# Performance work log

Measured on AMD Instinct MI355X. Metric: run time of the kernel, lower is better.

## Reference

```python
import jax, jax.numpy as jnp
import numpy as np

B, N, D = 8, 512, 768
HS = 64          # gp_head_size
NT = 12          # len(tag_vocab)
NEG = 1e12


def setup_inputs() -> dict:
    key = jax.random.key(0)
    ks = jax.random.split(key, 14)
    s = 0.02  # init scale for weights
    return {
        "chars": jax.random.normal(ks[0], (B, N, D), dtype=jnp.float32),
        "mask": jax.random.randint(ks[1], (B, N), 0, 2).astype(jnp.int32),
        "w1_ent": jax.random.normal(ks[2], (2 * HS, D), dtype=jnp.float32) * s,
        "b1_ent": jax.random.normal(ks[3], (2 * HS,), dtype=jnp.float32) * s,
        "w2_ent": jax.random.normal(ks[4], (2 * 2, 2 * HS), dtype=jnp.float32) * s,
        "b2_ent": jax.random.normal(ks[5], (2 * 2,), dtype=jnp.float32) * s,
        "w1_head": jax.random.normal(ks[6], (2 * HS, D), dtype=jnp.float32) * s,
        "b1_head": jax.random.normal(ks[7], (2 * HS,), dtype=jnp.float32) * s,
        "w2_head": jax.random.normal(ks[8], (2 * NT, 2 * HS), dtype=jnp.float32) * s,
        "b2_head": jax.random.normal(ks[9], (2 * NT,), dtype=jnp.float32) * s,
        "w1_tail": jax.random.normal(ks[10], (2 * HS, D), dtype=jnp.float32) * s,
        "b1_tail": jax.random.normal(ks[11], (2 * HS,), dtype=jnp.float32) * s,
        "w2_tail": jax.random.normal(ks[12], (2 * NT, 2 * HS), dtype=jnp.float32) * s,
        "b2_tail": jax.random.normal(ks[13], (2 * NT,), dtype=jnp.float32) * s,
    }


def _egp(x, w1, b1, w2, b2, mask, head_size, rope, tril):
    # x: [B,N,D] -> h: [B,N,2*head_size]
    h = jnp.einsum('bnd,ed->bne', x, w1) + b1
    qw, kw = h[..., 0::2], h[..., 1::2]          # [B,N,head_size] each
    if rope:
        n = x.shape[1]
        pos = jnp.arange(n, dtype=x.dtype)
        inv = jnp.power(10000.0, -2.0 * jnp.arange(head_size // 2, dtype=x.dtype) / head_size)
        ang = pos[:, None] * inv[None, :]         # [N, head_size/2]
        cos = jnp.repeat(jnp.cos(ang), 2, axis=-1)[None]  # [1,N,head_size]
        sin = jnp.repeat(jnp.sin(ang), 2, axis=-1)[None]
        def rot(t):
            t2 = jnp.stack([-t[..., 1::2], t[..., 0::2]], axis=-1).reshape(t.shape)
            return t * cos + t2 * sin
        qw, kw = rot(qw), rot(kw)
    logits = jnp.einsum('bmd,bnd->bmn', qw, kw) / (head_size ** 0.5)  # [B,M,N]
    bias = (jnp.einsum('bne,he->bnh', h, w2) + b2).transpose(0, 2, 1) / 2.0  # [B,2H,N]
    # [B,H,M,N]
    logits = logits[:, None] + bias[:, 0::2, None, :] + bias[:, 1::2, :, None]
    m = mask.astype(logits.dtype)
    pad = 1.0 - m[:, None, None, :] * m[:, None, :, None]
    logits = logits - pad * NEG
    if tril:
        tri = jnp.tril(jnp.ones((logits.shape[-2], logits.shape[-1]), logits.dtype), k=-1)
        logits = logits - tri * NEG
    return logits


def reference(chars, mask, w1_ent, b1_ent, w2_ent, b2_ent,
              w1_head, b1_head, w2_head, b2_head,
              w1_tail, b1_tail, w2_tail, b2_tail):
    entity = _egp(chars, w1_ent, b1_ent, w2_ent, b2_ent, mask, HS, True, True)
    head = _egp(chars, w1_head, b1_head, w2_head, b2_head, mask, HS, False, False)
    tail = _egp(chars, w1_tail, b1_tail, w2_tail, b2_tail, mask, HS, False, False)
    return (entity, head, tail)
```

## Files before the change

kernel.cpp:

```cpp
#include <hip/hip_runtime.h>
#include <cstddef>

namespace {
constexpr int B_ = 8;
constexpr int N_ = 512;
constexpr int D_ = 768;
constexpr int HS_ = 64;
constexpr int M_ = B_ * N_;
constexpr int E_ = 2 * HS_;
constexpr float NEGV = 1000000000000.0f;
constexpr float LOG2_10000 = 13.287712379549449f;
}

typedef short mfrag_t __attribute__((ext_vector_type(8)));
typedef float macc_t  __attribute__((ext_vector_type(4)));

__device__ __forceinline__ unsigned short bft(float x) {
    union { float f; unsigned u; } c; c.f = x;
    return (unsigned short)(c.u >> 16);
}
__device__ __forceinline__ unsigned short bfrne(float x) {
    union { float f; unsigned u; } c; c.f = x;
    const unsigned r = c.u + 0x7FFFu + ((c.u >> 16) & 1u);
    return (unsigned short)(r >> 16);
}

__global__ __launch_bounds__(256) void prep_kernel(
    const float* __restrict__ chars,
    const float* __restrict__ w1e, const float* __restrict__ b1e,
    const float* __restrict__ w2e, const float* __restrict__ b2e,
    const float* __restrict__ w1h, const float* __restrict__ b1h,
    const float* __restrict__ w2h, const float* __restrict__ b2h,
    const float* __restrict__ w1t, const float* __restrict__ b1t,
    const float* __restrict__ w2t, const float* __restrict__ b2t,
    unsigned short* __restrict__ qbf, unsigned short* __restrict__ kbf,
    float* __restrict__ bias_e, float* __restrict__ bias_h, float* __restrict__ bias_t)
{
    const int fam = blockIdx.y;
    const float* w1 = (fam == 0) ? w1e : (fam == 1) ? w1h : w1t;
    const float* b1 = (fam == 0) ? b1e : (fam == 1) ? b1h : b1t;
    const float* w2 = (fam == 0) ? w2e : (fam == 1) ? w2h : w2t;
    const float* b2 = (fam == 0) ? b2e : (fam == 1) ? b2h : b2t;
    float* bout = (fam == 0) ? bias_e : (fam == 1) ? bias_h : bias_t;
    const int H2 = (fam == 0) ? 4 : 24;
    unsigned short* qout = qbf + (size_t)fam * M_ * HS_;
    unsigned short* kout = kbf + (size_t)fam * M_ * HS_;
    const int m0 = blockIdx.x * 64;

    __shared__ unsigned short A_lds[64][40];
    __shared__ unsigned short B_lds[128][40];
    __shared__ float hs[64][132];

    const int t    = threadIdx.x;
    const int w    = t >> 6;
    const int lane = t & 63;
    const int ml   = lane & 15;
    const int quad = lane >> 4;

    const int ar = t >> 2;
    const int ak = (t & 3) * 8;
    const int bc = t >> 1;
    const int bk = (t & 1) * 16;

    const float* aptr = chars + (size_t)(m0 + ar) * D_ + ak;
    const float* bptr = w1 + (size_t)bc * D_ + bk;

    macc_t acc[8];
    #pragma unroll
    for (int f = 0; f < 8; ++f) acc[f] = (macc_t)0.0f;

    float4 av0 = *(const float4*)(aptr);
    float4 av1 = *(const float4*)(aptr + 4);
    float4 bv0 = *(const float4*)(bptr);
    float4 bv1 = *(const float4*)(bptr + 4);
    float4 bv2 = *(const float4*)(bptr + 8);
    float4 bv3 = *(const float4*)(bptr + 12);

    for (int s = 0; s < 24; ++s) {
        {
            mfrag_t pa;
            pa[0] = (short)bft(av0.x); pa[1] = (short)bft(av0.y);
            pa[2] = (short)bft(av0.z); pa[3] = (short)bft(av0.w);
            pa[4] = (short)bft(av1.x); pa[5] = (short)bft(av1.y);
            pa[6] = (short)bft(av1.z); pa[7] = (short)bft(av1.w);
            *(mfrag_t*)&A_lds[ar][ak] = pa;
            mfrag_t pb0, pb1;
            pb0[0] = (short)bft(bv0.x); pb0[1] = (short)bft(bv0.y);
            pb0[2] = (short)bft(bv0.z); pb0[3] = (short)bft(bv0.w);
            pb0[4] = (short)bft(bv1.x); pb0[5] = (short)bft(bv1.y);
            pb0[6] = (short)bft(bv1.z); pb0[7] = (short)bft(bv1.w);
            pb1[0] = (short)bft(bv2.x); pb1[1] = (short)bft(bv2.y);
            pb1[2] = (short)bft(bv2.z); pb1[3] = (short)bft(bv2.w);
            pb1[4] = (short)bft(bv3.x); pb1[5] = (short)bft(bv3.y);
            pb1[6] = (short)bft(bv3.z); pb1[7] = (short)bft(bv3.w);
            *(mfrag_t*)&B_lds[bc][bk]     = pb0;
            *(mfrag_t*)&B_lds[bc][bk + 8] = pb1;
        }
        __syncthreads();
        if (s < 23) {
            aptr += 32; bptr += 32;
            av0 = *(const float4*)(aptr);
            av1 = *(const float4*)(aptr + 4);
            bv0 = *(const float4*)(bptr);
            bv1 = *(const float4*)(bptr + 4);
            bv2 = *(const float4*)(bptr + 8);
            bv3 = *(const float4*)(bptr + 12);
        }
        const mfrag_t afrag = *(const mfrag_t*)&A_lds[w * 16 + ml][quad * 8];
        #pragma unroll
        for (int f = 0; f < 8; ++f) {
            const mfrag_t bfrag = *(const mfrag_t*)&B_lds[f * 16 + ml][quad * 8];
            acc[f] = __builtin_amdgcn_mfma_f32_16x16x32_bf16(afrag, bfrag, acc[f], 0, 0, 0);
        }
        __syncthreads();
    }

    #pragma unroll
    for (int f = 0; f < 8; ++f) {
        const int col = f * 16 + ml;
        const float bb1 = b1[col];
        #pragma unroll
        for (int r = 0; r < 4; ++r)
            hs[w * 16 + quad * 4 + r][col] = acc[f][r] + bb1;
    }
    __syncthreads();

    {
        const int row = t >> 2;
        const int kg  = t & 3;
        const float pos = (float)((m0 & 511) + row);
        unsigned short qv[16], kv[16];
        #pragma unroll
        for (int p = 0; p < 8; ++p) {
            const int i = kg * 8 + p;
            const float q0 = hs[row][4 * i + 0];
            const float k0 = hs[row][4 * i + 1];
            const float q1 = hs[row][4 * i + 2];
            const float k1 = hs[row][4 * i + 3];
            if (fam == 0) {
                const float inv = exp2f(-(float)i * (LOG2_10000 / 32.0f));
                float sn, cs;
                sincosf(pos * inv, &sn, &cs);
                qv[2 * p + 0] = bfrne(q0 * cs - q1 * sn);
                qv[2 * p + 1] = bfrne(q1 * cs + q0 * sn);
                kv[2 * p + 0] = bfrne(k0 * cs - k1 * sn);
                kv[2 * p + 1] = bfrne(k1 * cs + k0 * sn);
            } else {
                qv[2 * p + 0] = bfrne(q0);
                qv[2 * p + 1] = bfrne(q1);
                kv[2 * p + 0] = bfrne(k0);
                kv[2 * p + 1] = bfrne(k1);
            }
        }
        unsigned short* qp = qout + (size_t)(m0 + row) * HS_ + kg * 16;
        unsigned short* kp = kout + (size_t)(m0 + row) * HS_ + kg * 16;
        *(mfrag_t*)qp       = *(const mfrag_t*)&qv[0];
        *(mfrag_t*)(qp + 8) = *(const mfrag_t*)&qv[8];
        *(mfrag_t*)kp       = *(const mfrag_t*)&kv[0];
        *(mfrag_t*)(kp + 8) = *(const mfrag_t*)&kv[8];
    }

    {
        const int row = t & 63;
        const int h2b = t >> 6;
        const int P   = H2 >> 2;
        const int bb  = m0 >> 9;
        const int nb  = (m0 & 511) + row;
        float accv[6] = {0, 0, 0, 0, 0, 0};
        for (int e0 = 0; e0 < E_; e0 += 16) {
            float4 hv0 = *(const float4*)&hs[row][e0];
            float4 hv1 = *(const float4*)&hs[row][e0 + 4];
            float4 hv2 = *(const float4*)&hs[row][e0 + 8];
            float4 hv3 = *(const float4*)&hs[row][e0 + 12];
            for (int p = 0; p < P; ++p) {
                const float* wr = w2 + (size_t)(h2b + 4 * p) * E_ + e0;
                const float4 w0 = *(const float4*)(wr);
                const float4 w1v = *(const float4*)(wr + 4);
                const float4 w2v = *(const float4*)(wr + 8);
                const float4 w3v = *(const float4*)(wr + 12);
                accv[p] += hv0.x * w0.x + hv0.y * w0.y + hv0.z * w0.z + hv0.w * w0.w
                         + hv1.x * w1v.x + hv1.y * w1v.y + hv1.z * w1v.z + hv1.w * w1v.w
                         + hv2.x * w2v.x + hv2.y * w2v.y + hv2.z * w2v.z + hv2.w * w2v.w
                         + hv3.x * w3v.x + hv3.y * w3v.y + hv3.z * w3v.z + hv3.w * w3v.w;
            }
        }
        for (int p = 0; p < P; ++p) {
            const int h2 = h2b + 4 * p;
            bout[((size_t)bb * H2 + h2) * N_ + nb] = (accv[p] + b2[h2]) * 0.5f;
        }
    }
}

template <int H, bool TRIL>
__device__ __forceinline__ void egp_tile(
    const unsigned short* __restrict__ qf, const unsigned short* __restrict__ kf,
    const float* __restrict__ biasfam, const int* __restrict__ mask,
    float* __restrict__ out, int b, int m0, int n0, float (*Cs)[68], int t)
{
    const int w    = t >> 6;
    const int lane = t & 63;
    const int ml   = lane & 15;
    const int quad = lane >> 4;

    macc_t acc[4];
    #pragma unroll
    for (int f = 0; f < 4; ++f) acc[f] = (macc_t)0.0f;

    const unsigned short* qrow = qf + (size_t)(b * N_ + m0 + w * 16 + ml) * HS_ + quad * 8;
    const unsigned short* krow = kf + (size_t)(b * N_ + n0 + ml) * HS_ + quad * 8;

    #pragma unroll
    for (int s = 0; s < 2; ++s) {
        const mfrag_t af = *(const mfrag_t*)(qrow + s * 32);
        #pragma unroll
        for (int f = 0; f < 4; ++f) {
            const mfrag_t bf = *(const mfrag_t*)(krow + (size_t)f * 16 * HS_ + s * 32);
            acc[f] = __builtin_amdgcn_mfma_f32_16x16x32_bf16(af, bf, acc[f], 0, 0, 0);
        }
    }

    #pragma unroll
    for (int f = 0; f < 4; ++f)
        #pragma unroll
        for (int r = 0; r < 4; ++r)
            Cs[w * 16 + quad * 4 + r][f * 16 + ml] = acc[f][r] * 0.125f;
    __syncthreads();

    const int rq = t >> 4;
    const int cq = t & 15;

    float4 av[4];
    #pragma unroll
    for (int j = 0; j < 4; ++j) av[j] = *(const float4*)&Cs[4 * rq + j][4 * cq];

    int mrow[4], mm[4];
    #pragma unroll
    for (int j = 0; j < 4; ++j) {
        mrow[j] = m0 + 4 * rq + j;
        mm[j]   = mask[b * N_ + mrow[j]];
    }
    const int ncol = n0 + 4 * cq;
    const int4 mnv = *(const int4*)(mask + b * N_ + ncol);
    const int mn[4] = { mnv.x, mnv.y, mnv.z, mnv.w };

    #pragma unroll
    for (int hh = 0; hh < H; ++hh) {
        const float4 be = *(const float4*)(biasfam + ((size_t)b * 2 * H + 2 * hh) * N_ + ncol);
        float bo[4];
        #pragma unroll
        for (int j = 0; j < 4; ++j)
            bo[j] = biasfam[((size_t)b * 2 * H + 2 * hh + 1) * N_ + mrow[j]];

        #pragma unroll
        for (int j = 0; j < 4; ++j) {
            const float* aj = (const float*)&av[j];
            float o[4] = { aj[0] + be.x + bo[j], aj[1] + be.y + bo[j],
                           aj[2] + be.z + bo[j], aj[3] + be.w + bo[j] };
            #pragma unroll
            for (int q = 0; q < 4; ++q) {
                if (!(mm[j] & mn[q])) o[q] -= NEGV;
                if (TRIL && (ncol + q) < mrow[j]) o[q] -= NEGV;
            }
            *(float4*)(out + ((size_t)(b * H + hh) * N_ + mrow[j]) * N_ + ncol) =
                make_float4(o[0], o[1], o[2], o[3]);
        }
    }
}

__global__ __launch_bounds__(256) void egp_all_kernel(
    const unsigned short* __restrict__ qbf, const unsigned short* __restrict__ kbf,
    const float* __restrict__ bias_e, const float* __restrict__ bias_h,
    const float* __restrict__ bias_t,
    const int* __restrict__ mask, float* __restrict__ out)
{
    __shared__ float Cs[64][68];

    const int t   = threadIdx.x;
    const int m0  = blockIdx.x * 64;
    const int n0  = blockIdx.y * 64;
    const int fam = blockIdx.z >> 3;
    const int b   = blockIdx.z & 7;

    const size_t ent_sz  = (size_t)B_ * 2 * N_ * N_;
    const size_t head_sz = (size_t)B_ * 12 * N_ * N_;
    const size_t fsl = (size_t)M_ * HS_;

    if (fam == 0) {
        egp_tile<2, true>(qbf, kbf, bias_e, mask, out, b, m0, n0, Cs, t);
    } else if (fam == 1) {
        egp_tile<12, false>(qbf + fsl, kbf + fsl, bias_h, mask,
                            out + ent_sz, b, m0, n0, Cs, t);
    } else {
        egp_tile<12, false>(qbf + 2 * fsl, kbf + 2 * fsl, bias_t, mask,
                            out + ent_sz + head_sz, b, m0, n0, Cs, t);
    }
}

extern "C" void kernel_launch(void* const* d_in, const int* in_sizes, int n_in,
                              void* d_out, int out_size, void* d_ws, size_t ws_size,
                              hipStream_t stream)
{
    const float* chars = (const float*)d_in[0];
    const int*   mask  = (const int*)d_in[1];
    const float* w1e = (const float*)d_in[2];
    const float* b1e = (const float*)d_in[3];
    const float* w2e = (const float*)d_in[4];
    const float* b2e = (const float*)d_in[5];
    const float* w1h = (const float*)d_in[6];
    const float* b1h = (const float*)d_in[7];
    const float* w2h = (const float*)d_in[8];
    const float* b2h = (const float*)d_in[9];
    const float* w1t = (const float*)d_in[10];
    const float* b1t = (const float*)d_in[11];
    const float* w2t = (const float*)d_in[12];
    const float* b2t = (const float*)d_in[13];

    float* out = (float*)d_out;

    unsigned short* qbf = (unsigned short*)d_ws;
    unsigned short* kbf = qbf + (size_t)3 * M_ * HS_;
    float* bias_e = (float*)(kbf + (size_t)3 * M_ * HS_);
    float* bias_h = bias_e + (size_t)B_ * 4 * N_;
    float* bias_t = bias_h + (size_t)B_ * 24 * N_;

    prep_kernel<<<dim3(64, 3), 256, 0, stream>>>(
        chars, w1e, b1e, w2e, b2e, w1h, b1h, w2h, b2h, w1t, b1t, w2t, b2t,
        qbf, kbf, bias_e, bias_h, bias_t);

    egp_all_kernel<<<dim3(8, 8, 24), 256, 0, stream>>>(
        qbf, kbf, bias_e, bias_h, bias_t, mask, out);
}
```

Baseline: 283.9 us.

## Halve prep row tile to double blocks and use nontemporal output stores

New measurement: 283.1 us. No clear change (-0.3%).

```diff
diff --git a/kernel.cpp b/kernel.cpp
--- a/kernel.cpp
+++ b/kernel.cpp
@@ -13,7 +13,9 @@
 }
 
 typedef short mfrag_t __attribute__((ext_vector_type(8)));
+typedef short mhalf_t __attribute__((ext_vector_type(4)));
 typedef float macc_t  __attribute__((ext_vector_type(4)));
+typedef float vf4_t   __attribute__((ext_vector_type(4)));
 
 __device__ __forceinline__ unsigned short bft(float x) {
     union { float f; unsigned u; } c; c.f = x;
@@ -45,32 +47,33 @@
     const int H2 = (fam == 0) ? 4 : 24;
     unsigned short* qout = qbf + (size_t)fam * M_ * HS_;
     unsigned short* kout = kbf + (size_t)fam * M_ * HS_;
-    const int m0 = blockIdx.x * 64;
-
-    __shared__ unsigned short A_lds[64][40];
+    const int m0 = blockIdx.x * 32;
+
+    __shared__ unsigned short A_lds[32][40];
     __shared__ unsigned short B_lds[128][40];
-    __shared__ float hs[64][132];
+    __shared__ float hs[32][132];
 
     const int t    = threadIdx.x;
     const int w    = t >> 6;
     const int lane = t & 63;
     const int ml   = lane & 15;
     const int quad = lane >> 4;
-
-    const int ar = t >> 2;
-    const int ak = (t & 3) * 8;
+    const int wr16 = (w & 1) * 16;
+    const int wc64 = (w >> 1) * 64;
+
+    const int ar = t >> 3;
+    const int ak = (t & 7) * 4;
     const int bc = t >> 1;
     const int bk = (t & 1) * 16;
 
     const float* aptr = chars + (size_t)(m0 + ar) * D_ + ak;
     const float* bptr = w1 + (size_t)bc * D_ + bk;
 
-    macc_t acc[8];
-    #pragma unroll
-    for (int f = 0; f < 8; ++f) acc[f] = (macc_t)0.0f;
+    macc_t acc[4];
+    #pragma unroll
+    for (int f = 0; f < 4; ++f) acc[f] = (macc_t)0.0f;
 
     float4 av0 = *(const float4*)(aptr);
-    float4 av1 = *(const float4*)(aptr + 4);
     float4 bv0 = *(const float4*)(bptr);
     float4 bv1 = *(const float4*)(bptr + 4);
     float4 bv2 = *(const float4*)(bptr + 8);
@@ -78,12 +81,10 @@
 
     for (int s = 0; s < 24; ++s) {
         {
-            mfrag_t pa;
+            mhalf_t pa;
             pa[0] = (short)bft(av0.x); pa[1] = (short)bft(av0.y);
             pa[2] = (short)bft(av0.z); pa[3] = (short)bft(av0.w);
-            pa[4] = (short)bft(av1.x); pa[5] = (short)bft(av1.y);
-            pa[6] = (short)bft(av1.z); pa[7] = (short)bft(av1.w);
-            *(mfrag_t*)&A_lds[ar][ak] = pa;
+            *(mhalf_t*)&A_lds[ar][ak] = pa;
             mfrag_t pb0, pb1;
             pb0[0] = (short)bft(bv0.x); pb0[1] = (short)bft(bv0.y);
             pb0[2] = (short)bft(bv0.z); pb0[3] = (short)bft(bv0.w);
@@ -100,39 +101,38 @@
         if (s < 23) {
             aptr += 32; bptr += 32;
             av0 = *(const float4*)(aptr);
-            av1 = *(const float4*)(aptr + 4);
             bv0 = *(const float4*)(bptr);
             bv1 = *(const float4*)(bptr + 4);
             bv2 = *(const float4*)(bptr + 8);
             bv3 = *(const float4*)(bptr + 12);
         }
-        const mfrag_t afrag = *(const mfrag_t*)&A_lds[w * 16 + ml][quad * 8];
-        #pragma unroll
-        for (int f = 0; f < 8; ++f) {
-            const mfrag_t bfrag = *(const mfrag_t*)&B_lds[f * 16 + ml][quad * 8];
+        const mfrag_t afrag = *(const mfrag_t*)&A_lds[wr16 + ml][quad * 8];
+        #pragma unroll
+        for (int f = 0; f < 4; ++f) {
+            const mfrag_t bfrag = *(const mfrag_t*)&B_lds[wc64 + f * 16 + ml][quad * 8];
             acc[f] = __builtin_amdgcn_mfma_f32_16x16x32_bf16(afrag, bfrag, acc[f], 0, 0, 0);
         }
         __syncthreads();
     }
 
     #pragma unroll
-    for (int f = 0; f < 8; ++f) {
-        const int col = f * 16 + ml;
+    for (int f = 0; f < 4; ++f) {
+        const int col = wc64 + f * 16 + ml;
         const float bb1 = b1[col];
         #pragma unroll
         for (int r = 0; r < 4; ++r)
-            hs[w * 16 + quad * 4 + r][col] = acc[f][r] + bb1;
+            hs[wr16 + quad * 4 + r][col] = acc[f][r] + bb1;
     }
     __syncthreads();
 
     {
-        const int row = t >> 2;
-        const int kg  = t & 3;
+        const int row = t >> 3;
+        const int kg  = t & 7;
         const float pos = (float)((m0 & 511) + row);
-        unsigned short qv[16], kv[16];
-        #pragma unroll
-        for (int p = 0; p < 8; ++p) {
-            const int i = kg * 8 + p;
+        unsigned short qv[8], kv[8];
+        #pragma unroll
+        for (int p = 0; p < 4; ++p) {
+            const int i = kg * 4 + p;
             const float q0 = hs[row][4 * i + 0];
             const float k0 = hs[row][4 * i + 1];
             const float q1 = hs[row][4 * i + 2];
@@ -152,28 +152,26 @@
                 kv[2 * p + 1] = bfrne(k1);
             }
         }
-        unsigned short* qp = qout + (size_t)(m0 + row) * HS_ + kg * 16;
-        unsigned short* kp = kout + (size_t)(m0 + row) * HS_ + kg * 16;
-        *(mfrag_t*)qp       = *(const mfrag_t*)&qv[0];
-        *(mfrag_t*)(qp + 8) = *(const mfrag_t*)&qv[8];
-        *(mfrag_t*)kp       = *(const mfrag_t*)&kv[0];
-        *(mfrag_t*)(kp + 8) = *(const mfrag_t*)&kv[8];
+        unsigned short* qp = qout + (size_t)(m0 + row) * HS_ + kg * 8;
+        unsigned short* kp = kout + (size_t)(m0 + row) * HS_ + kg * 8;
+        *(mfrag_t*)qp = *(const mfrag_t*)&qv[0];
+        *(mfrag_t*)kp = *(const mfrag_t*)&kv[0];
     }
 
     {
-        const int row = t & 63;
-        const int h2b = t >> 6;
-        const int P   = H2 >> 2;
+        const int row = t & 31;
+        const int h2b = t >> 5;
         const int bb  = m0 >> 9;
         const int nb  = (m0 & 511) + row;
-        float accv[6] = {0, 0, 0, 0, 0, 0};
+        float accv[3] = {0, 0, 0};
         for (int e0 = 0; e0 < E_; e0 += 16) {
             float4 hv0 = *(const float4*)&hs[row][e0];
             float4 hv1 = *(const float4*)&hs[row][e0 + 4];
             float4 hv2 = *(const float4*)&hs[row][e0 + 8];
             float4 hv3 = *(const float4*)&hs[row][e0 + 12];
-            for (int p = 0; p < P; ++p) {
-                const float* wr = w2 + (size_t)(h2b + 4 * p) * E_ + e0;
+            int p = 0;
+            for (int h2 = h2b; h2 < H2; h2 += 8, ++p) {
+                const float* wr = w2 + (size_t)h2 * E_ + e0;
                 const float4 w0 = *(const float4*)(wr);
                 const float4 w1v = *(const float4*)(wr + 4);
                 const float4 w2v = *(const float4*)(wr + 8);
@@ -184,10 +182,9 @@
                          + hv3.x * w3v.x + hv3.y * w3v.y + hv3.z * w3v.z + hv3.w * w3v.w;
             }
         }
-        for (int p = 0; p < P; ++p) {
-            const int h2 = h2b + 4 * p;
+        int p = 0;
+        for (int h2 = h2b; h2 < H2; h2 += 8, ++p)
             bout[((size_t)bb * H2 + h2) * N_ + nb] = (accv[p] + b2[h2]) * 0.5f;
-        }
     }
 }
 
@@ -261,8 +258,10 @@
                 if (!(mm[j] & mn[q])) o[q] -= NEGV;
                 if (TRIL && (ncol + q) < mrow[j]) o[q] -= NEGV;
             }
-            *(float4*)(out + ((size_t)(b * H + hh) * N_ + mrow[j]) * N_ + ncol) =
-                make_float4(o[0], o[1], o[2], o[3]);
+            vf4_t ov;
+            ov.x = o[0]; ov.y = o[1]; ov.z = o[2]; ov.w = o[3];
+            __builtin_nontemporal_store(
+                ov, (vf4_t*)(out + ((size_t)(b * H + hh) * N_ + mrow[j]) * N_ + ncol));
         }
     }
 }
@@ -323,7 +322,7 @@
     float* bias_h = bias_e + (size_t)B_ * 4 * N_;
     float* bias_t = bias_h + (size_t)B_ * 24 * N_;
 
-    prep_kernel<<<dim3(64, 3), 256, 0, stream>>>(
+    prep_kernel<<<dim3(128, 3), 256, 0, stream>>>(
         chars, w1e, b1e, w2e, b2e, w1h, b1h, w2h, b2h, w1t, b1t, w2t, b2t,
         qbf, kbf, bias_e, bias_h, bias_t);
 
```
